# Optimization experiments

Hardware: AMD Instinct MI355X
Metric: run time of the kernel (lower is better)

## Reference

```python
import jax, jax.numpy as jnp
import numpy as np

B, S, D, H = 2, 2048, 768, 12
DK = D // H


def setup_inputs() -> dict:
    key = jax.random.key(0)
    ks = jax.random.split(key, 10)
    sc = 0.02
    return {
        "k": jax.random.normal(ks[0], (B, S, D), jnp.float32),
        "q": jax.random.normal(ks[1], (B, S, D), jnp.float32),
        "v": jax.random.normal(ks[2], (B, S, D), jnp.float32),
        "mask": jnp.ones((B, 1, S, S), jnp.int32),
        "wq": jax.random.normal(ks[3], (D, D), jnp.float32) * sc,
        "bq": jnp.zeros((D,), jnp.float32),
        "wk": jax.random.normal(ks[4], (D, D), jnp.float32) * sc,
        "bk": jnp.zeros((D,), jnp.float32),
        "wv": jax.random.normal(ks[5], (D, D), jnp.float32) * sc,
        "bv": jnp.zeros((D,), jnp.float32),
        "wo": jax.random.normal(ks[6], (D, D), jnp.float32) * sc,
        "bo": jnp.zeros((D,), jnp.float32),
    }


def reference(k, q, v, mask, wq, bq, wk, bk, wv, bv, wo, bo):
    # Linear projections (torch Linear: x @ W^T + b)
    query = q @ wq.T + bq
    key_ = k @ wk.T + bk
    value = v @ wv.T + bv
    # [B,S,D] -> [B,H,S,DK]
    def split_heads(x):
        return x.reshape(B, S, H, DK).transpose(0, 2, 1, 3)
    Q, K, V = split_heads(query), split_heads(key_), split_heads(value)
    # NOTE: original masked_fill result is discarded -> mask is a no-op.
    scores = jnp.einsum("bhqd,bhkd->bhqk", Q, K) / jnp.sqrt(jnp.float32(DK))
    attn = jax.nn.softmax(scores, axis=-1)  # dropout p=0.0 -> identity
    out = jnp.einsum("bhqk,bhkd->bhqd", attn, V)
    out = out.transpose(0, 2, 1, 3).reshape(B, S, D)
    return out @ wo.T + bo
```

## Files before the change

### kernel.cpp

```cpp
#include <hip/hip_runtime.h>
#include <hip/hip_bf16.h>

#define B_  2
#define S_  2048
#define D_  768
#define H_  12
#define DK_ 64
#define NX_ (B_*S_*D_)
#define NW_ (D_*D_)
#define CSC 0.18033688011112042f

typedef __attribute__((ext_vector_type(8))) short  bf16x8;
typedef __attribute__((ext_vector_type(4))) float  f32x4;

__device__ __forceinline__ unsigned short f2bf(float f) {
    unsigned int u = __float_as_uint(f);
    u += 0x7fffu + ((u >> 16) & 1u);
    return (unsigned short)(u >> 16);
}

__device__ __forceinline__ unsigned pack_bf2(float a, float b) {
    const unsigned ua = __float_as_uint(a) + 0x8000u;
    const unsigned ub = __float_as_uint(b) + 0x8000u;
    return __builtin_amdgcn_perm(ub, ua, 0x07060302u);
}

__device__ __forceinline__ void async_cp16(const unsigned short* g,
                                           const unsigned short* lds_uniform_base) {
    __builtin_amdgcn_global_load_lds(
        (const __attribute__((address_space(1))) unsigned int*)(uintptr_t)g,
        (__attribute__((address_space(3))) unsigned int*)(unsigned int)(uintptr_t)lds_uniform_base,
        16, 0, 0);
}

struct CvtArgs { const float* s[7]; };

__global__ __launch_bounds__(256) void cvt_all(CvtArgs a,
                                               unsigned short* __restrict__ Xsw,
                                               unsigned short* __restrict__ Wsw) {
    const int bx = blockIdx.x;
    int y, inner;
    if (bx < 2304) { y = bx / 768;             inner = bx % 768; }
    else           { y = 3 + (bx - 2304) / 144; inner = (bx - 2304) % 144; }
    const int idx = inner * 256 + threadIdx.x;
    const int n  = idx / 48;
    const int g2 = idx % 48;
    const float* src = a.s[y] + (long)n * D_ + g2 * 16;
    const float zs = (y == 3) ? CSC : 1.0f;
    unsigned short o[16];
#pragma unroll
    for (int i = 0; i < 4; i++) {
        const float4 f = *(const float4*)(src + i * 4);
        o[i*4+0] = f2bf(f.x*zs); o[i*4+1] = f2bf(f.y*zs);
        o[i*4+2] = f2bf(f.z*zs); o[i*4+3] = f2bf(f.w*zs);
    }
    unsigned short* dst = (y >= 3) ? (Wsw + (long)(y - 3) * NW_ + (long)n * D_)
                                   : (Xsw + (long)y * NX_ + (long)n * D_);
    const int key = n & 7;
#pragma unroll
    for (int h = 0; h < 2; h++) {
        const int g8 = g2 * 2 + h;
        const int kdst = (g8 >> 3) * 64 + (((g8 & 7) ^ key) * 8);
        *(uint4*)(dst + kdst) = *(const uint4*)&o[h * 8];
    }
}

struct QkvArgs { const float* bias[3]; unsigned short* out[3]; };

__global__ __launch_bounds__(256, 3) void gemm_qkv(QkvArgs args,
                                                   const unsigned short* __restrict__ Xsw,
                                                   const unsigned short* __restrict__ Wsw) {
    __shared__ __align__(16) unsigned short smem[17408];
    unsigned short* As = smem;
    unsigned short* Bs = smem + 8192;

    const int t    = threadIdx.x;
    const int wave = t >> 6;
    const int lane = t & 63;
    const int l16  = lane & 15;
    const int quad = lane >> 4;
    const int wm   = wave >> 1, wn = wave & 1;
    const int m0   = blockIdx.x * 128;
    const int zz   = blockIdx.y / 6;
    const int nb   = blockIdx.y % 6;
    const int n0   = nb * 128;

    const unsigned short* Ap = Xsw + (long)zz * NX_;
    const unsigned short* Wp = Wsw + (long)zz * NW_;

    f32x4 acc[4][4];
#pragma unroll
    for (int s = 0; s < 4; s++)
#pragma unroll
        for (int j = 0; j < 4; j++) acc[s][j] = (f32x4){0.f, 0.f, 0.f, 0.f};

    const int lrow = lane >> 3;
    const int lcg  = lane & 7;

    for (int k0 = 0; k0 < D_; k0 += 64) {
        __syncthreads();
#pragma unroll
        for (int i = 0; i < 4; i++) {
            const int chunk = wave * 4 + i;
            async_cp16(Ap + (long)(m0 + chunk * 8 + lrow) * D_ + k0 + lcg * 8,
                       As + chunk * 512);
        }
#pragma unroll
        for (int i = 0; i < 4; i++) {
            const int chunk = wave * 4 + i;
            async_cp16(Wp + (long)(n0 + chunk * 8 + lrow) * D_ + k0 + lcg * 8,
                       Bs + chunk * 512);
        }
        __syncthreads();
#pragma unroll
        for (int ks = 0; ks < 2; ks++) {
            const int cg = ks * 4 + quad;
            bf16x8 af[4], bf[4];
#pragma unroll
            for (int s = 0; s < 4; s++) {
                const int r = wm * 64 + s * 16 + l16;
                af[s] = *(const bf16x8*)&As[r * 64 + ((cg ^ (r & 7)) * 8)];
            }
#pragma unroll
            for (int j = 0; j < 4; j++) {
                const int r = wn * 64 + j * 16 + l16;
                bf[j] = *(const bf16x8*)&Bs[r * 64 + ((cg ^ (r & 7)) * 8)];
            }
#pragma unroll
            for (int s = 0; s < 4; s++)
#pragma unroll
                for (int j = 0; j < 4; j++)
                    acc[s][j] = __builtin_amdgcn_mfma_f32_16x16x32_bf16(af[s], bf[j], acc[s][j], 0, 0, 0);
        }
    }
    __syncthreads();

    const int b     = m0 >> 11;
    const int sbase = m0 & (S_ - 1);
    const float zs  = (zz == 0) ? CSC : 1.0f;
    float bv[4];
#pragma unroll
    for (int j = 0; j < 4; j++) bv[j] = args.bias[zz][n0 + wn * 64 + j * 16 + l16] * zs;

    if (zz < 2) {
        unsigned short* Ls = smem;
#pragma unroll
        for (int s = 0; s < 4; s++)
#pragma unroll
            for (int j = 0; j < 4; j++)
#pragma unroll
                for (int r = 0; r < 4; r++)
                    Ls[(wm * 64 + s * 16 + quad * 4 + r) * 136 + wn * 64 + j * 16 + l16] =
                        f2bf(acc[s][j][r] + bv[j]);
        __syncthreads();
        const int row  = t >> 1;
        const int half = t & 1;
        unsigned short* Op = args.out[zz];
#pragma unroll
        for (int i = 0; i < 8; i++) {
            const int col  = half * 64 + i * 8;
            const int head = nb * 2 + half;
            const uint4 v = *(const uint4*)&Ls[row * 136 + col];
            *(uint4*)(Op + ((long)(b * H_ + head) * S_ + sbase + row) * DK_ + (col & 63)) = v;
        }
    } else {
        unsigned short* Ls = smem;
#pragma unroll
        for (int s = 0; s < 4; s++)
#pragma unroll
            for (int j = 0; j < 4; j++)
#pragma unroll
                for (int r = 0; r < 4; r++) {
                    const int dk  = j * 16 + l16;
                    const int pos = wm * 64 + (quad * 4 + r) * 4 + s;
                    Ls[wn * 8704 + dk * 136 + pos] = f2bf(acc[s][j][r] + bv[j]);
                }
        __syncthreads();
        const int rowIdx = t >> 1;
        const int hh = rowIdx >> 6, dk = rowIdx & 63;
        const int half = t & 1;
        unsigned short* Op = args.out[2];
#pragma unroll
        for (int i = 0; i < 8; i++) {
            const int col = half * 64 + i * 8;
            const uint4 v = *(const uint4*)&Ls[hh * 8704 + dk * 136 + col];
            const int head = nb * 2 + hh;
            *(uint4*)(Op + ((long)(b * H_ + head) * DK_ + dk) * S_ + sbase + col) = v;
        }
    }
}

__global__ __launch_bounds__(256, 2) void attn_kernel(
    const unsigned short* __restrict__ Q, const unsigned short* __restrict__ K,
    const unsigned short* __restrict__ Vt, unsigned short* __restrict__ Ao)
{
    const int t    = threadIdx.x;
    const int wave = t >> 6;
    const int lane = t & 63;
    const int l16  = lane & 15;
    const int quad = lane >> 4;
    const int bid  = blockIdx.x;
    const int bh    = bid % 24;
    const int qtile = bid / 24;

    const unsigned short* Qp = Q  + (long)bh * S_ * DK_;
    const unsigned short* Kp = K  + (long)bh * S_ * DK_;
    const unsigned short* Vp = Vt + (long)bh * DK_ * S_;

    __shared__ __align__(16) unsigned short smem[24576];
    unsigned short* Ps = smem + 16384;

    const int fkey = l16 & 7;
    const int fo0  = (((0 * 4 + quad) ^ fkey) * 8);
    const int fo1  = (((1 * 4 + quad) ^ fkey) * 8);

    bf16x8 qf[2][2];
#pragma unroll
    for (int rb = 0; rb < 2; rb++) {
        const long qoff = (long)(qtile * 128 + wave * 32 + rb * 16 + l16) * DK_ + quad * 8;
        qf[rb][0] = *(const bf16x8*)(Qp + qoff);
        qf[rb][1] = *(const bf16x8*)(Qp + qoff + 32);
    }

    const int srow = t >> 2;
    const int sc2  = t & 3;
    const int skey = srow & 7;
    const int sA   = srow * 64 + (((2 * sc2)     ^ skey) * 8);
    const int sB   = srow * 64 + (((2 * sc2 + 1) ^ skey) * 8);
    uint4 kreg[2], vreg[2];
    const unsigned short* gk = Kp + (long)srow * DK_ + sc2 * 16;
    const unsigned short* gv = Vp + (long)srow * S_ + sc2 * 16;
    kreg[0] = *(const uint4*)gk;  kreg[1] = *(const uint4*)(gk + 8);
    vreg[0] = *(const uint4*)gv;  vreg[1] = *(const uint4*)(gv + 8);
    gk += 64 * DK_;  gv += 64;
    *(uint4*)&smem[sA]        = kreg[0];
    *(uint4*)&smem[sB]        = kreg[1];
    *(uint4*)&smem[8192 + sA] = vreg[0];
    *(uint4*)&smem[8192 + sB] = vreg[1];

    f32x4 oacc[2][4];
#pragma unroll
    for (int rb = 0; rb < 2; rb++)
#pragma unroll
        for (int j = 0; j < 4; j++) oacc[rb][j] = (f32x4){0.f, 0.f, 0.f, 0.f};
    float lsum[2][4] = {{0.f,0.f,0.f,0.f},{0.f,0.f,0.f,0.f}};

    for (int it = 0; it < 32; ++it) {
        const int co = (it & 1) * 4096;
        const int no = 4096 - co;
        __syncthreads();
        const unsigned short* Ks = smem + co;
        const unsigned short* Vs = smem + 8192 + co;

        if (it < 31) {
            kreg[0] = *(const uint4*)gk;  kreg[1] = *(const uint4*)(gk + 8);
            vreg[0] = *(const uint4*)gv;  vreg[1] = *(const uint4*)(gv + 8);
            gk += 64 * DK_;  gv += 64;
        }

#pragma unroll
        for (int rb = 0; rb < 2; rb++) {
            f32x4 sacc[4];
#pragma unroll
            for (int j = 0; j < 4; j++) sacc[j] = (f32x4){0.f, 0.f, 0.f, 0.f};
#pragma unroll
            for (int j = 0; j < 4; j++) {
                const bf16x8 bf0 = *(const bf16x8*)&Ks[(j * 16 + l16) * 64 + fo0];
                sacc[j] = __builtin_amdgcn_mfma_f32_16x16x32_bf16(qf[rb][0], bf0, sacc[j], 0, 0, 0);
                const bf16x8 bf1 = *(const bf16x8*)&Ks[(j * 16 + l16) * 64 + fo1];
                sacc[j] = __builtin_amdgcn_mfma_f32_16x16x32_bf16(qf[rb][1], bf1, sacc[j], 0, 0, 0);
            }
#pragma unroll
            for (int r = 0; r < 4; r++) {
                const float p0 = exp2f(sacc[0][r]);
                const float p1 = exp2f(sacc[1][r]);
                const float p2 = exp2f(sacc[2][r]);
                const float p3 = exp2f(sacc[3][r]);
                lsum[rb][r] += (p0 + p1) + (p2 + p3);
                uint2 pk = {pack_bf2(p0, p1), pack_bf2(p2, p3)};
                const int prow = wave * 32 + rb * 16 + quad * 4 + r;
                const int padr = prow * 64 + (((l16 >> 1) ^ ((quad * 4 + r) & 7)) * 8)
                               + (l16 & 1) * 4;
                *(uint2*)&Ps[padr] = pk;
            }
        }

#pragma unroll
        for (int rb = 0; rb < 2; rb++) {
#pragma unroll
            for (int ks = 0; ks < 2; ks++) {
                const int fo = ks ? fo1 : fo0;
                const bf16x8 pf = *(const bf16x8*)&Ps[(wave * 32 + rb * 16 + l16) * 64 + fo];
#pragma unroll
                for (int j = 0; j < 4; j++) {
                    const bf16x8 vf = *(const bf16x8*)&Vs[(j * 16 + l16) * 64 + fo];
                    oacc[rb][j] = __builtin_amdgcn_mfma_f32_16x16x32_bf16(pf, vf, oacc[rb][j], 0, 0, 0);
                }
            }
        }

        if (it < 31) {
            *(uint4*)&smem[no + sA]        = kreg[0];
            *(uint4*)&smem[no + sB]        = kreg[1];
            *(uint4*)&smem[8192 + no + sA] = vreg[0];
            *(uint4*)&smem[8192 + no + sB] = vreg[1];
        }
    }

#pragma unroll
    for (int rb = 0; rb < 2; rb++)
#pragma unroll
        for (int r = 0; r < 4; r++) {
#pragma unroll
            for (int off = 1; off < 16; off <<= 1)
                lsum[rb][r] += __shfl_xor(lsum[rb][r], off, 64);
            lsum[rb][r] = 1.f / lsum[rb][r];
        }

    __syncthreads();
#pragma unroll
    for (int rb = 0; rb < 2; rb++)
#pragma unroll
        for (int j = 0; j < 4; j++)
#pragma unroll
            for (int r = 0; r < 4; r++) {
                const int row = wave * 32 + rb * 16 + quad * 4 + r;
                const int key = (quad * 4 + r) & 7;
                const int c   = j * 2 + (l16 >> 3);
                Ps[row * 64 + ((c ^ key) * 8) + (l16 & 7)] =
                    f2bf(oacc[rb][j][r] * lsum[rb][r]);
            }

    const int row  = t >> 1;
    const int qrow = qtile * 128 + row;
    const int b = bh / H_, h = bh % H_;
    unsigned short* dst = Ao + (long)(b * S_ + qrow) * D_ + h * DK_;
#pragma unroll
    for (int i = 0; i < 4; i++) {
        const int p = (t & 1) * 4 + i;
        *(uint4*)(dst + p * 8) = *(const uint4*)&Ps[row * 64 + p * 8];
    }
}

__global__ __launch_bounds__(256, 4) void gemm_out(
    const unsigned short* __restrict__ A, const unsigned short* __restrict__ Wsw,
    const float* __restrict__ bias, float* __restrict__ Out)
{
    __shared__ __align__(16) unsigned short smem[8704];
    unsigned short* As = smem;
    unsigned short* Bs = smem + 4096;

    const int t    = threadIdx.x;
    const int wave = t >> 6;
    const int lane = t & 63;
    const int l16  = lane & 15;
    const int quad = lane >> 4;
    const int wm   = wave >> 1, wn = wave & 1;
    const int m0   = blockIdx.x * 64;
    const int n0   = blockIdx.y * 64;

    f32x4 acc[2][2];
#pragma unroll
    for (int s = 0; s < 2; s++)
#pragma unroll
        for (int j = 0; j < 2; j++) acc[s][j] = (f32x4){0.f, 0.f, 0.f, 0.f};

    const int lrow = lane >> 3;
    const int lcg  = lane & 7;

    for (int k0 = 0; k0 < D_; k0 += 64) {
        __syncthreads();
#pragma unroll
        for (int i = 0; i < 2; i++) {
            const int chunk = wave * 2 + i;
            async_cp16(A + (long)(m0 + chunk * 8 + lrow) * D_ + k0 + lcg * 8,
                       As + chunk * 512);
        }
#pragma unroll
        for (int i = 0; i < 2; i++) {
            const int chunk = wave * 2 + i;
            async_cp16(Wsw + (long)(n0 + chunk * 8 + lrow) * D_ + k0 + lcg * 8,
                       Bs + chunk * 512);
        }
        __syncthreads();
#pragma unroll
        for (int ks = 0; ks < 2; ks++) {
            const int cg = ks * 4 + quad;
            bf16x8 af[2], bf[2];
#pragma unroll
            for (int s = 0; s < 2; s++) {
                const int r = wm * 32 + s * 16 + l16;
                af[s] = *(const bf16x8*)&As[r * 64 + ((cg ^ (r & 7)) * 8)];
            }
#pragma unroll
            for (int j = 0; j < 2; j++) {
                const int r = wn * 32 + j * 16 + l16;
                bf[j] = *(const bf16x8*)&Bs[r * 64 + ((cg ^ (r & 7)) * 8)];
            }
#pragma unroll
            for (int s = 0; s < 2; s++)
#pragma unroll
                for (int j = 0; j < 2; j++)
                    acc[s][j] = __builtin_amdgcn_mfma_f32_16x16x32_bf16(af[s], bf[j], acc[s][j], 0, 0, 0);
        }
    }

    float bv[2];
#pragma unroll
    for (int j = 0; j < 2; j++) bv[j] = bias[n0 + wn * 32 + j * 16 + l16];

    __syncthreads();
    float* fl = (float*)smem;
#pragma unroll
    for (int s = 0; s < 2; s++)
#pragma unroll
        for (int j = 0; j < 2; j++)
#pragma unroll
            for (int r = 0; r < 4; r++)
                fl[(wm * 32 + s * 16 + quad * 4 + r) * 67 + wn * 32 + j * 16 + l16] =
                    acc[s][j][r] + bv[j];
    __syncthreads();
    const int row = t >> 2, c0 = (t & 3) * 16;
#pragma unroll
    for (int i = 0; i < 4; i++) {
        const float4 v = *(const float4*)&fl[row * 67 + c0 + i * 4];
        *(float4*)(Out + (long)(m0 + row) * D_ + n0 + c0 + i * 4) = v;
    }
}

extern "C" void kernel_launch(void* const* d_in, const int* in_sizes, int n_in,
                              void* d_out, int out_size, void* d_ws, size_t ws_size,
                              hipStream_t stream) {
    const float* k_in = (const float*)d_in[0];
    const float* q_in = (const float*)d_in[1];
    const float* v_in = (const float*)d_in[2];
    const float* wq = (const float*)d_in[4];
    const float* bq = (const float*)d_in[5];
    const float* wk = (const float*)d_in[6];
    const float* bk = (const float*)d_in[7];
    const float* wv = (const float*)d_in[8];
    const float* bv = (const float*)d_in[9];
    const float* wo = (const float*)d_in[10];
    const float* bo = (const float*)d_in[11];

    unsigned short* ws = (unsigned short*)d_ws;
    unsigned short* Wsw = ws;
    unsigned short* Qb  = Wsw + 4ll * NW_;
    unsigned short* Kb  = Qb + (long)NX_;
    unsigned short* Vt  = Kb + (long)NX_;
    unsigned short* Xsw = Vt + (long)NX_;
    unsigned short* Ao  = Xsw;

    CvtArgs ca;
    ca.s[0] = q_in; ca.s[1] = k_in; ca.s[2] = v_in;
    ca.s[3] = wq;   ca.s[4] = wk;   ca.s[5] = wv;  ca.s[6] = wo;
    cvt_all<<<dim3(2880), 256, 0, stream>>>(ca, Xsw, Wsw);

    QkvArgs qa;
    qa.bias[0] = bq; qa.bias[1] = bk; qa.bias[2] = bv;
    qa.out[0] = Qb;  qa.out[1] = Kb;  qa.out[2] = Vt;
    gemm_qkv<<<dim3(32, 18), 256, 0, stream>>>(qa, Xsw, Wsw);

    attn_kernel<<<dim3(384), 256, 0, stream>>>(Qb, Kb, Vt, Ao);

    gemm_out<<<dim3(64, 12), 256, 0, stream>>>(Ao, Wsw + 3ll * NW_, bo, (float*)d_out);
}
```

Measured before the change: 225.8 us.

## Halve attention block to 64 query rows and hoist K/V fragment loads

The attention kernel now uses 128-thread blocks covering 64 query rows, launched as 768 blocks instead of 384, so more workgroups are spread across the CUs. Each thread stages twice as many K/V bytes per tile, and shared memory drops because the P buffer shrinks. K and V MFMA fragments are loaded once per tile into registers and reused across both row blocks, instead of being reloaded inside the row-block loop. The trade-off is that each K/V tile is now read from global memory by twice as many blocks, and register pressure rises.

```diff
diff --git a/kernel.cpp b/kernel.cpp
--- a/kernel.cpp
+++ b/kernel.cpp
@@ -190,7 +190,7 @@
     }
 }
 
-__global__ __launch_bounds__(256, 2) void attn_kernel(
+__global__ __launch_bounds__(128, 2) void attn_kernel(
     const unsigned short* __restrict__ Q, const unsigned short* __restrict__ K,
     const unsigned short* __restrict__ Vt, unsigned short* __restrict__ Ao)
 {
@@ -207,36 +207,40 @@
     const unsigned short* Kp = K  + (long)bh * S_ * DK_;
     const unsigned short* Vp = Vt + (long)bh * DK_ * S_;
 
-    __shared__ __align__(16) unsigned short smem[24576];
+    __shared__ __align__(16) unsigned short smem[20480];
     unsigned short* Ps = smem + 16384;
 
     const int fkey = l16 & 7;
-    const int fo0  = (((0 * 4 + quad) ^ fkey) * 8);
-    const int fo1  = (((1 * 4 + quad) ^ fkey) * 8);
+    const int fo0  = ((quad ^ fkey) * 8);
+    const int fo1  = (((4 + quad) ^ fkey) * 8);
 
     bf16x8 qf[2][2];
 #pragma unroll
     for (int rb = 0; rb < 2; rb++) {
-        const long qoff = (long)(qtile * 128 + wave * 32 + rb * 16 + l16) * DK_ + quad * 8;
+        const long qoff = (long)(qtile * 64 + wave * 32 + rb * 16 + l16) * DK_ + quad * 8;
         qf[rb][0] = *(const bf16x8*)(Qp + qoff);
         qf[rb][1] = *(const bf16x8*)(Qp + qoff + 32);
     }
 
-    const int srow = t >> 2;
-    const int sc2  = t & 3;
-    const int skey = srow & 7;
-    const int sA   = srow * 64 + (((2 * sc2)     ^ skey) * 8);
-    const int sB   = srow * 64 + (((2 * sc2 + 1) ^ skey) * 8);
-    uint4 kreg[2], vreg[2];
-    const unsigned short* gk = Kp + (long)srow * DK_ + sc2 * 16;
-    const unsigned short* gv = Vp + (long)srow * S_ + sc2 * 16;
-    kreg[0] = *(const uint4*)gk;  kreg[1] = *(const uint4*)(gk + 8);
-    vreg[0] = *(const uint4*)gv;  vreg[1] = *(const uint4*)(gv + 8);
+    const int srow  = t >> 1;
+    const int shalf = t & 1;
+    const int skey  = srow & 7;
+    int sOff[4];
+#pragma unroll
+    for (int i = 0; i < 4; i++) {
+        const int c = shalf * 4 + i;
+        sOff[i] = srow * 64 + ((c ^ skey) * 8);
+    }
+    uint4 kreg[4], vreg[4];
+    const unsigned short* gk = Kp + (long)srow * DK_ + shalf * 32;
+    const unsigned short* gv = Vp + (long)srow * S_ + shalf * 32;
+#pragma unroll
+    for (int i = 0; i < 4; i++) { kreg[i] = *(const uint4*)(gk + i * 8);
+                                  vreg[i] = *(const uint4*)(gv + i * 8); }
     gk += 64 * DK_;  gv += 64;
-    *(uint4*)&smem[sA]        = kreg[0];
-    *(uint4*)&smem[sB]        = kreg[1];
-    *(uint4*)&smem[8192 + sA] = vreg[0];
-    *(uint4*)&smem[8192 + sB] = vreg[1];
+#pragma unroll
+    for (int i = 0; i < 4; i++) { *(uint4*)&smem[sOff[i]]        = kreg[i];
+                                  *(uint4*)&smem[8192 + sOff[i]] = vreg[i]; }
 
     f32x4 oacc[2][4];
 #pragma unroll
@@ -253,57 +257,70 @@
         const unsigned short* Vs = smem + 8192 + co;
 
         if (it < 31) {
-            kreg[0] = *(const uint4*)gk;  kreg[1] = *(const uint4*)(gk + 8);
-            vreg[0] = *(const uint4*)gv;  vreg[1] = *(const uint4*)(gv + 8);
+#pragma unroll
+            for (int i = 0; i < 4; i++) { kreg[i] = *(const uint4*)(gk + i * 8);
+                                          vreg[i] = *(const uint4*)(gv + i * 8); }
             gk += 64 * DK_;  gv += 64;
         }
 
-#pragma unroll
-        for (int rb = 0; rb < 2; rb++) {
-            f32x4 sacc[4];
-#pragma unroll
-            for (int j = 0; j < 4; j++) sacc[j] = (f32x4){0.f, 0.f, 0.f, 0.f};
-#pragma unroll
-            for (int j = 0; j < 4; j++) {
-                const bf16x8 bf0 = *(const bf16x8*)&Ks[(j * 16 + l16) * 64 + fo0];
-                sacc[j] = __builtin_amdgcn_mfma_f32_16x16x32_bf16(qf[rb][0], bf0, sacc[j], 0, 0, 0);
-                const bf16x8 bf1 = *(const bf16x8*)&Ks[(j * 16 + l16) * 64 + fo1];
-                sacc[j] = __builtin_amdgcn_mfma_f32_16x16x32_bf16(qf[rb][1], bf1, sacc[j], 0, 0, 0);
-            }
+        bf16x8 kf[2][4];
+#pragma unroll
+        for (int j = 0; j < 4; j++) {
+            kf[0][j] = *(const bf16x8*)&Ks[(j * 16 + l16) * 64 + fo0];
+            kf[1][j] = *(const bf16x8*)&Ks[(j * 16 + l16) * 64 + fo1];
+        }
+
+        f32x4 sacc[2][4];
+#pragma unroll
+        for (int rb = 0; rb < 2; rb++)
+#pragma unroll
+            for (int j = 0; j < 4; j++) sacc[rb][j] = (f32x4){0.f, 0.f, 0.f, 0.f};
+#pragma unroll
+        for (int rb = 0; rb < 2; rb++)
+#pragma unroll
+            for (int ks = 0; ks < 2; ks++)
+#pragma unroll
+                for (int j = 0; j < 4; j++)
+                    sacc[rb][j] = __builtin_amdgcn_mfma_f32_16x16x32_bf16(
+                        qf[rb][ks], kf[ks][j], sacc[rb][j], 0, 0, 0);
+
+#pragma unroll
+        for (int rb = 0; rb < 2; rb++)
 #pragma unroll
             for (int r = 0; r < 4; r++) {
-                const float p0 = exp2f(sacc[0][r]);
-                const float p1 = exp2f(sacc[1][r]);
-                const float p2 = exp2f(sacc[2][r]);
-                const float p3 = exp2f(sacc[3][r]);
+                const float p0 = exp2f(sacc[rb][0][r]);
+                const float p1 = exp2f(sacc[rb][1][r]);
+                const float p2 = exp2f(sacc[rb][2][r]);
+                const float p3 = exp2f(sacc[rb][3][r]);
                 lsum[rb][r] += (p0 + p1) + (p2 + p3);
                 uint2 pk = {pack_bf2(p0, p1), pack_bf2(p2, p3)};
                 const int prow = wave * 32 + rb * 16 + quad * 4 + r;
-                const int padr = prow * 64 + (((l16 >> 1) ^ ((quad * 4 + r) & 7)) * 8)
-                               + (l16 & 1) * 4;
-                *(uint2*)&Ps[padr] = pk;
-            }
-        }
-
-#pragma unroll
-        for (int rb = 0; rb < 2; rb++) {
+                *(uint2*)&Ps[prow * 64 + (((l16 >> 1) ^ (prow & 7)) * 8) + (l16 & 1) * 4] = pk;
+            }
+
+        bf16x8 vf[2][4];
+#pragma unroll
+        for (int j = 0; j < 4; j++) {
+            vf[0][j] = *(const bf16x8*)&Vs[(j * 16 + l16) * 64 + fo0];
+            vf[1][j] = *(const bf16x8*)&Vs[(j * 16 + l16) * 64 + fo1];
+        }
+
+#pragma unroll
+        for (int rb = 0; rb < 2; rb++)
 #pragma unroll
             for (int ks = 0; ks < 2; ks++) {
                 const int fo = ks ? fo1 : fo0;
                 const bf16x8 pf = *(const bf16x8*)&Ps[(wave * 32 + rb * 16 + l16) * 64 + fo];
 #pragma unroll
-                for (int j = 0; j < 4; j++) {
-                    const bf16x8 vf = *(const bf16x8*)&Vs[(j * 16 + l16) * 64 + fo];
-                    oacc[rb][j] = __builtin_amdgcn_mfma_f32_16x16x32_bf16(pf, vf, oacc[rb][j], 0, 0, 0);
-                }
-            }
-        }
+                for (int j = 0; j < 4; j++)
+                    oacc[rb][j] = __builtin_amdgcn_mfma_f32_16x16x32_bf16(
+                        pf, vf[ks][j], oacc[rb][j], 0, 0, 0);
+            }
 
         if (it < 31) {
-            *(uint4*)&smem[no + sA]        = kreg[0];
-            *(uint4*)&smem[no + sB]        = kreg[1];
-            *(uint4*)&smem[8192 + no + sA] = vreg[0];
-            *(uint4*)&smem[8192 + no + sB] = vreg[1];
+#pragma unroll
+            for (int i = 0; i < 4; i++) { *(uint4*)&smem[no + sOff[i]]        = kreg[i];
+                                          *(uint4*)&smem[8192 + no + sOff[i]] = vreg[i]; }
         }
     }
 
@@ -325,19 +342,18 @@
 #pragma unroll
             for (int r = 0; r < 4; r++) {
                 const int row = wave * 32 + rb * 16 + quad * 4 + r;
-                const int key = (quad * 4 + r) & 7;
                 const int c   = j * 2 + (l16 >> 3);
-                Ps[row * 64 + ((c ^ key) * 8) + (l16 & 7)] =
+                Ps[row * 64 + ((c ^ (row & 7)) * 8) + (l16 & 7)] =
                     f2bf(oacc[rb][j][r] * lsum[rb][r]);
             }
 
+    const int b = bh / H_, h = bh % H_;
     const int row  = t >> 1;
-    const int qrow = qtile * 128 + row;
-    const int b = bh / H_, h = bh % H_;
+    const int qrow = qtile * 64 + row;
     unsigned short* dst = Ao + (long)(b * S_ + qrow) * D_ + h * DK_;
 #pragma unroll
     for (int i = 0; i < 4; i++) {
-        const int p = (t & 1) * 4 + i;
+        const int p = shalf * 4 + i;
         *(uint4*)(dst + p * 8) = *(const uint4*)&Ps[row * 64 + p * 8];
     }
 }
@@ -461,7 +477,7 @@
     qa.out[0] = Qb;  qa.out[1] = Kb;  qa.out[2] = Vt;
     gemm_qkv<<<dim3(32, 18), 256, 0, stream>>>(qa, Xsw, Wsw);
 
-    attn_kernel<<<dim3(384), 256, 0, stream>>>(Qb, Kb, Vt, Ao);
+    attn_kernel<<<dim3(768), 128, 0, stream>>>(Qb, Kb, Vt, Ao);
 
     gemm_out<<<dim3(64, 12), 256, 0, stream>>>(Ao, Wsw + 3ll * NW_, bo, (float*)d_out);
 }
```

New measurement: 222.0 us. Within noise of the previous version (-1.7%).
